# Kernel optimization log

Hardware: AMD Instinct MI355X
Metric: run time of the kernel (lower is better)

Reference implementation:

```python
import jax, jax.numpy as jnp
import numpy as np

N_USER = 100000
N_ITEM = 50000
N_NODES = N_USER + N_ITEM
LATDIM = 64
N_EDGES = 4800000
N_LAYERS = 3


def setup_inputs() -> dict:
    key = jax.random.key(0)
    k1, k2, k3, k4 = jax.random.split(key, 4)
    ini_embeds = jax.random.normal(k1, (N_NODES, LATDIM), dtype=jnp.float32)
    edge_src = jax.random.randint(k2, (N_EDGES,), 0, N_NODES, dtype=jnp.int32)
    edge_dst = jax.random.randint(k3, (N_EDGES,), 0, N_NODES, dtype=jnp.int32)
    edge_w = jax.random.uniform(k4, (N_EDGES,), dtype=jnp.float32)
    return {
        "ini_embeds": ini_embeds,
        "edge_src": edge_src,
        "edge_dst": edge_dst,
        "edge_w": edge_w,
        "n_user": N_USER,
        "n_layers": N_LAYERS,
    }


def _spmm(edge_src, edge_dst, edge_w, x, n_nodes):
    # out[dst] += w * x[src]  == adj @ x for sparse adj in COO form
    msgs = x[edge_src] * edge_w[:, None]  # [E, D]
    return jax.ops.segment_sum(msgs, edge_dst, num_segments=n_nodes)


def reference(ini_embeds, edge_src, edge_dst, edge_w, n_user, n_layers):
    n_nodes = ini_embeds.shape[0]
    embeds = ini_embeds
    acc = ini_embeds  # running sum of all layer embeddings (LightGCN layer sum)
    for _ in range(n_layers):
        embeds = _spmm(edge_src, edge_dst, edge_w, embeds, n_nodes)
        acc = acc + embeds
    return acc[:n_user], acc[n_user:]
```

## Files before the change

kernel.cpp:

```cpp
#include <hip/hip_runtime.h>
#include <hip/hip_fp16.h>


#define D 64
#define BSH 9
#define BW 512
#define PTILE 16384

__global__ void lg_zero_int(int* __restrict__ p, int n) {
    int i = blockIdx.x * blockDim.x + threadIdx.x;
    int st = gridDim.x * blockDim.x;
    for (; i < n; i += st) p[i] = 0;
}

__global__ void lg_f2h(const float* __restrict__ in, __half* __restrict__ out, int n4) {
    int i = blockIdx.x * blockDim.x + threadIdx.x;
    int st = gridDim.x * blockDim.x;
    const float4* src = (const float4*)in;
    uint2* dst = (uint2*)out;
    for (; i < n4; i += st) {
        float4 v = src[i];
        __half2 a = __floats2half2_rn(v.x, v.y);
        __half2 b = __floats2half2_rn(v.z, v.w);
        uint2 u;
        u.x = *reinterpret_cast<unsigned int*>(&a);
        u.y = *reinterpret_cast<unsigned int*>(&b);
        dst[i] = u;
    }
}

__global__ void lg_bhist(const int* __restrict__ edst, int* __restrict__ bcount,
                         int E, int NB) {
    extern __shared__ int lcnt[];
    for (int i = threadIdx.x; i < NB; i += blockDim.x) lcnt[i] = 0;
    __syncthreads();
    int i = blockIdx.x * blockDim.x + threadIdx.x;
    int st = gridDim.x * blockDim.x;
    for (; i < E; i += st) atomicAdd(&lcnt[edst[i] >> BSH], 1);
    __syncthreads();
    for (int j = threadIdx.x; j < NB; j += blockDim.x) {
        int v = lcnt[j];
        if (v) atomicAdd(&bcount[j], v);
    }
}

__global__ __launch_bounds__(1024) void lg_bscan(const int* counts, int* bptr, int* bcur,
                                                 int NB, int E, int* rowptr, int n_nodes) {
    __shared__ int lds[1024];
    int tid = threadIdx.x;
    int per = (NB + 1023) >> 10;
    int lo = tid * per; if (lo > NB) lo = NB;
    int hi = lo + per;  if (hi > NB) hi = NB;
    int sum = 0;
    for (int i = lo; i < hi; ++i) sum += counts[i];
    lds[tid] = sum;
    __syncthreads();
    for (int off = 1; off < 1024; off <<= 1) {
        int v = (tid >= off) ? lds[tid - off] : 0;
        __syncthreads();
        lds[tid] += v;
        __syncthreads();
    }
    int run = lds[tid] - sum;
    for (int i = lo; i < hi; ++i) {
        int c = counts[i];
        bptr[i] = run;
        bcur[i] = run;
        run += c;
    }
    if (tid == 0) { bptr[NB] = E; rowptr[n_nodes] = E; }
}

__global__ __launch_bounds__(256) void lg_part(const int* __restrict__ esrc,
                                               const int* __restrict__ edst,
                                               const float* __restrict__ ew,
                                               int* __restrict__ bcur,
                                               int2* __restrict__ bbuf,
                                               int E, int NB) {
    extern __shared__ int sm[];
    int* cnt = sm;
    int* base = sm + NB;
    int lo = blockIdx.x * PTILE;
    int hi = lo + PTILE; if (hi > E) hi = E;
    for (int i = threadIdx.x; i < NB; i += 256) cnt[i] = 0;
    __syncthreads();
    for (int i = lo + threadIdx.x; i < hi; i += 256)
        atomicAdd(&cnt[edst[i] >> BSH], 1);
    __syncthreads();
    for (int i = threadIdx.x; i < NB; i += 256) {
        int c = cnt[i];
        base[i] = c ? atomicAdd(&bcur[i], c) : 0;
        cnt[i] = 0;
    }
    __syncthreads();
    for (int i = lo + threadIdx.x; i < hi; i += 256) {
        int d = edst[i];
        int b = d >> BSH;
        int p = base[b] + atomicAdd(&cnt[b], 1);
        bbuf[p] = make_int2(esrc[i] | ((d & (BW - 1)) << 18), __float_as_int(ew[i]));
    }
}

__global__ __launch_bounds__(256) void lg_bfinal(const int2* __restrict__ bbuf,
                                                 const int* __restrict__ bptr,
                                                 int2* __restrict__ edata,
                                                 int* __restrict__ rowptr, int n_nodes) {
    __shared__ int cnt[BW];
    __shared__ int cur[BW];
    __shared__ int psum[256];
    int b = blockIdx.x;
    int s = bptr[b], e = bptr[b + 1];
    int tid = threadIdx.x;
    for (int i = tid; i < BW; i += 256) cnt[i] = 0;
    __syncthreads();
    for (int i = s + tid; i < e; i += 256)
        atomicAdd(&cnt[((unsigned)bbuf[i].x >> 18) & (BW - 1)], 1);
    __syncthreads();
    int c0 = cnt[2 * tid], c1 = cnt[2 * tid + 1];
    int mysum = c0 + c1;
    psum[tid] = mysum;
    __syncthreads();
    for (int off = 1; off < 256; off <<= 1) {
        int v = (tid >= off) ? psum[tid - off] : 0;
        __syncthreads();
        psum[tid] += v;
        __syncthreads();
    }
    int excl = psum[tid] - mysum;
    cur[2 * tid] = excl;
    cur[2 * tid + 1] = excl + c0;
    int node0 = b * BW + 2 * tid;
    if (node0 < n_nodes)     rowptr[node0]     = s + excl;
    if (node0 + 1 < n_nodes) rowptr[node0 + 1] = s + excl + c0;
    __syncthreads();
    for (int i = s + tid; i < e; i += 256) {
        int2 ed = bbuf[i];
        int loc = ((unsigned)ed.x >> 18) & (BW - 1);
        int p = s + atomicAdd(&cur[loc], 1);
        edata[p] = make_int2(ed.x & 0x3FFFF, ed.y);
    }
}

template <bool FIRST, bool LAST>
__global__ __launch_bounds__(256) void lg_gather(const int2* __restrict__ edata,
                                                 const int* __restrict__ rowptr,
                                                 const __half* __restrict__ x,
                                                 __half* __restrict__ y,
                                                 float* __restrict__ acc,
                                                 const float* __restrict__ ini,
                                                 int n_nodes) {
    int wid = (blockIdx.x * blockDim.x + threadIdx.x) >> 6;
    int lane = threadIdx.x & 63;
    if (wid >= n_nodes) return;
    int q = lane >> 4, c = lane & 15;
    int start = rowptr[wid], end = rowptr[wid + 1];
    float ax = 0.f, ay = 0.f, az = 0.f, aw = 0.f;
    int base = start;
    for (; base + 16 <= end; base += 16) {
        int2 e0 = edata[base + q];
        int2 e1 = edata[base + 4 + q];
        int2 e2 = edata[base + 8 + q];
        int2 e3 = edata[base + 12 + q];
        uint2 u0 = *((const uint2*)(x + (size_t)e0.x * D) + c);
        uint2 u1 = *((const uint2*)(x + (size_t)e1.x * D) + c);
        uint2 u2 = *((const uint2*)(x + (size_t)e2.x * D) + c);
        uint2 u3 = *((const uint2*)(x + (size_t)e3.x * D) + c);
        float w0 = __int_as_float(e0.y), w1 = __int_as_float(e1.y);
        float w2 = __int_as_float(e2.y), w3 = __int_as_float(e3.y);
        {
            float2 f0 = __half22float2(*reinterpret_cast<__half2*>(&u0.x));
            float2 f1 = __half22float2(*reinterpret_cast<__half2*>(&u0.y));
            ax += w0 * f0.x; ay += w0 * f0.y; az += w0 * f1.x; aw += w0 * f1.y;
        }
        {
            float2 f0 = __half22float2(*reinterpret_cast<__half2*>(&u1.x));
            float2 f1 = __half22float2(*reinterpret_cast<__half2*>(&u1.y));
            ax += w1 * f0.x; ay += w1 * f0.y; az += w1 * f1.x; aw += w1 * f1.y;
        }
        {
            float2 f0 = __half22float2(*reinterpret_cast<__half2*>(&u2.x));
            float2 f1 = __half22float2(*reinterpret_cast<__half2*>(&u2.y));
            ax += w2 * f0.x; ay += w2 * f0.y; az += w2 * f1.x; aw += w2 * f1.y;
        }
        {
            float2 f0 = __half22float2(*reinterpret_cast<__half2*>(&u3.x));
            float2 f1 = __half22float2(*reinterpret_cast<__half2*>(&u3.y));
            ax += w3 * f0.x; ay += w3 * f0.y; az += w3 * f1.x; aw += w3 * f1.y;
        }
    }
    for (; base < end; base += 4) {
        int idx = base + q;
        if (idx < end) {
            int2 e0 = edata[idx];
            float w0 = __int_as_float(e0.y);
            uint2 u0 = *((const uint2*)(x + (size_t)e0.x * D) + c);
            float2 f0 = __half22float2(*reinterpret_cast<__half2*>(&u0.x));
            float2 f1 = __half22float2(*reinterpret_cast<__half2*>(&u0.y));
            ax += w0 * f0.x; ay += w0 * f0.y; az += w0 * f1.x; aw += w0 * f1.y;
        }
    }
    ax += __shfl_xor(ax, 16); ax += __shfl_xor(ax, 32);
    ay += __shfl_xor(ay, 16); ay += __shfl_xor(ay, 32);
    az += __shfl_xor(az, 16); az += __shfl_xor(az, 32);
    aw += __shfl_xor(aw, 16); aw += __shfl_xor(aw, 32);
    if (lane < 16) {
        size_t o = (size_t)wid * D + (size_t)c * 4;
        if (!LAST) {
            __half2 h0 = __floats2half2_rn(ax, ay);
            __half2 h1 = __floats2half2_rn(az, aw);
            uint2 u;
            u.x = *reinterpret_cast<unsigned int*>(&h0);
            u.y = *reinterpret_cast<unsigned int*>(&h1);
            *(uint2*)(y + o) = u;
        }
        if (FIRST) {
            float4 iv = *(const float4*)(ini + o);
            *(float4*)(acc + o) = make_float4(iv.x + ax, iv.y + ay, iv.z + az, iv.w + aw);
        } else {
            float4 av = *(float4*)(acc + o);
            *(float4*)(acc + o) = make_float4(av.x + ax, av.y + ay, av.z + az, av.w + aw);
        }
    }
}

__global__ void lg_init_kernel(const float* __restrict__ ini, float* __restrict__ cur,
                               float* __restrict__ acc, float* __restrict__ nxt, int n4) {
    int i = blockIdx.x * blockDim.x + threadIdx.x;
    int stride = gridDim.x * blockDim.x;
    const float4* s = (const float4*)ini;
    float4* c = (float4*)cur; float4* a = (float4*)acc; float4* z = (float4*)nxt;
    float4 zero = make_float4(0.f, 0.f, 0.f, 0.f);
    for (; i < n4; i += stride) { float4 v = s[i]; c[i] = v; a[i] = v; z[i] = zero; }
}

__global__ void lg_spmm_kernel(const int* __restrict__ esrc, const int* __restrict__ edst,
                               const float* __restrict__ ew, const float* __restrict__ x,
                               float* __restrict__ y, int E) {
    int tid = blockIdx.x * blockDim.x + threadIdx.x;
    int e = tid >> 4;
    if (e >= E) return;
    int l = (tid & 15) << 2;
    int s = esrc[e]; int d = edst[e]; float w = ew[e];
    float4 v = *(const float4*)(x + s * D + l);
    float* yp = y + d * D + l;
    unsafeAtomicAdd(yp + 0, w * v.x);
    unsafeAtomicAdd(yp + 1, w * v.y);
    unsafeAtomicAdd(yp + 2, w * v.z);
    unsafeAtomicAdd(yp + 3, w * v.w);
}

__global__ void lg_addzero_kernel(float* __restrict__ acc, const float* __restrict__ nxt,
                                  float* __restrict__ zbuf, int n4) {
    int i = blockIdx.x * blockDim.x + threadIdx.x;
    int stride = gridDim.x * blockDim.x;
    float4* a = (float4*)acc; const float4* n = (const float4*)nxt; float4* z = (float4*)zbuf;
    float4 zero = make_float4(0.f, 0.f, 0.f, 0.f);
    for (; i < n4; i += stride) {
        float4 av = a[i]; float4 nv = n[i];
        av.x += nv.x; av.y += nv.y; av.z += nv.z; av.w += nv.w;
        a[i] = av; z[i] = zero;
    }
}

extern "C" void kernel_launch(void* const* d_in, const int* in_sizes, int n_in,
                              void* d_out, int out_size, void* d_ws, size_t ws_size,
                              hipStream_t stream) {
    const float* ini  = (const float*)d_in[0];
    const int*   esrc = (const int*)d_in[1];
    const int*   edst = (const int*)d_in[2];
    const float* ew   = (const float*)d_in[3];

    int n_nodes = in_sizes[0] / D;
    int E       = in_sizes[1];
    int NB      = (n_nodes + BW - 1) >> BSH;

    size_t hBytes     = ((size_t)n_nodes * D * sizeof(__half) + 255) & ~(size_t)255;
    size_t edataBytes = (size_t)E * sizeof(int2);
    size_t ptrBytes   = (((size_t)n_nodes + 1) * 4 + 15) & ~(size_t)15;
    size_t bptrBytes  = (((size_t)NB + 1) * 4 + 15) & ~(size_t)15;
    size_t need = 2 * hBytes + 2 * edataBytes + ptrBytes + bptrBytes + (size_t)NB * 4 + 64;

    float* acc = (float*)d_out;

    if (ws_size >= need) {
        char* p = (char*)d_ws;
        __half* h0    = (__half*)p; p += hBytes;
        __half* h1    = (__half*)p; p += hBytes;
        int2*  edata  = (int2*)p;   p += edataBytes;
        int2*  bbuf   = (int2*)p;   p += edataBytes;
        int*   rowptr = (int*)p;    p += ptrBytes;
        int*   bptr   = (int*)p;    p += bptrBytes;
        int*   bcur   = (int*)p;

        int ntiles = (E + PTILE - 1) / PTILE;
        int n4 = n_nodes * D / 4;

        lg_zero_int<<<(NB + 255) / 256, 256, 0, stream>>>(bcur, NB);
        lg_bhist<<<256, 256, (size_t)NB * 4, stream>>>(edst, bcur, E, NB);
        lg_bscan<<<1, 1024, 0, stream>>>(bcur, bptr, bcur, NB, E, rowptr, n_nodes);
        lg_part<<<ntiles, 256, (size_t)NB * 8, stream>>>(esrc, edst, ew, bcur, bbuf, E, NB);
        lg_f2h<<<2048, 256, 0, stream>>>(ini, h0, n4);
        lg_bfinal<<<NB, 256, 0, stream>>>(bbuf, bptr, edata, rowptr, n_nodes);

        int gblocks = (int)(((size_t)n_nodes * 64 + 255) / 256);
        lg_gather<true,  false><<<gblocks, 256, 0, stream>>>(edata, rowptr, h0, h1, acc, ini, n_nodes);
        lg_gather<false, false><<<gblocks, 256, 0, stream>>>(edata, rowptr, h1, h0, acc, ini, n_nodes);
        lg_gather<false, true ><<<gblocks, 256, 0, stream>>>(edata, rowptr, h0, h1, acc, ini, n_nodes);
    } else {
        int n4 = (n_nodes * D) / 4;
        float* cur = (float*)d_ws;
        float* nxt = cur + (size_t)n_nodes * D;
        lg_init_kernel<<<2048, 256, 0, stream>>>(ini, cur, acc, nxt, n4);
        int spmm_blocks = (E * 16 + 255) / 256;
        for (int layer = 0; layer < 3; ++layer) {
            lg_spmm_kernel<<<spmm_blocks, 256, 0, stream>>>(esrc, edst, ew, cur, nxt, E);
            lg_addzero_kernel<<<2048, 256, 0, stream>>>(acc, nxt, cur, n4);
            float* t = cur; cur = nxt; nxt = t;
        }
    }
}
```

Before: 487.7 us.

## Replace global-atomic bucket partition with per-tile histogram and flat scan

Rebuilds the CSR construction as a deterministic per-tile-per-bucket histogram, followed by one flat exclusive scan over an NB×ntiles table and a scatter that takes its offsets straight from that table. This removes the zeroing kernel, the global bucket-count atomics, and the per-tile global atomicAdd on bucket cursors. Block sizes go up to 1024 threads, and the final sort-within-bucket uses 512 scan lanes. In exchange, a single block must scan about 294×293 ≈ 86K entries, and the histogram table takes extra global memory traffic.

```diff
diff --git a/kernel.cpp b/kernel.cpp
--- a/kernel.cpp
+++ b/kernel.cpp
@@ -6,12 +6,6 @@
 #define BSH 9
 #define BW 512
 #define PTILE 16384
-
-__global__ void lg_zero_int(int* __restrict__ p, int n) {
-    int i = blockIdx.x * blockDim.x + threadIdx.x;
-    int st = gridDim.x * blockDim.x;
-    for (; i < n; i += st) p[i] = 0;
-}
 
 __global__ void lg_f2h(const float* __restrict__ in, __half* __restrict__ out, int n4) {
     int i = blockIdx.x * blockDim.x + threadIdx.x;
@@ -29,30 +23,33 @@
     }
 }
 
-__global__ void lg_bhist(const int* __restrict__ edst, int* __restrict__ bcount,
-                         int E, int NB) {
-    extern __shared__ int lcnt[];
-    for (int i = threadIdx.x; i < NB; i += blockDim.x) lcnt[i] = 0;
-    __syncthreads();
-    int i = blockIdx.x * blockDim.x + threadIdx.x;
-    int st = gridDim.x * blockDim.x;
-    for (; i < E; i += st) atomicAdd(&lcnt[edst[i] >> BSH], 1);
-    __syncthreads();
-    for (int j = threadIdx.x; j < NB; j += blockDim.x) {
-        int v = lcnt[j];
-        if (v) atomicAdd(&bcount[j], v);
-    }
-}
-
-__global__ __launch_bounds__(1024) void lg_bscan(const int* counts, int* bptr, int* bcur,
-                                                 int NB, int E, int* rowptr, int n_nodes) {
+__global__ __launch_bounds__(1024) void lg_tilehist(const int* __restrict__ edst,
+                                                    int* __restrict__ tcnt,
+                                                    int E, int NB, int ntiles) {
+    extern __shared__ int cnt[];
+    int t = blockIdx.x;
+    int lo = t * PTILE;
+    int hi = lo + PTILE; if (hi > E) hi = E;
+    for (int i = threadIdx.x; i < NB; i += 1024) cnt[i] = 0;
+    __syncthreads();
+    for (int i = lo + threadIdx.x; i < hi; i += 1024)
+        atomicAdd(&cnt[edst[i] >> BSH], 1);
+    __syncthreads();
+    for (int b = threadIdx.x; b < NB; b += 1024)
+        tcnt[b * ntiles + t] = cnt[b];
+}
+
+__global__ __launch_bounds__(1024) void lg_flatscan(const int* __restrict__ tcnt,
+                                                    int* __restrict__ tbase,
+                                                    int NT, int E,
+                                                    int* __restrict__ rowptr, int n_nodes) {
     __shared__ int lds[1024];
     int tid = threadIdx.x;
-    int per = (NB + 1023) >> 10;
-    int lo = tid * per; if (lo > NB) lo = NB;
-    int hi = lo + per;  if (hi > NB) hi = NB;
+    int per = (NT + 1023) >> 10;
+    int lo = tid * per; if (lo > NT) lo = NT;
+    int hi = lo + per;  if (hi > NT) hi = NT;
     int sum = 0;
-    for (int i = lo; i < hi; ++i) sum += counts[i];
+    for (int i = lo; i < hi; ++i) sum += tcnt[i];
     lds[tid] = sum;
     __syncthreads();
     for (int off = 1; off < 1024; off <<= 1) {
@@ -63,77 +60,66 @@
     }
     int run = lds[tid] - sum;
     for (int i = lo; i < hi; ++i) {
-        int c = counts[i];
-        bptr[i] = run;
-        bcur[i] = run;
-        run += c;
-    }
-    if (tid == 0) { bptr[NB] = E; rowptr[n_nodes] = E; }
-}
-
-__global__ __launch_bounds__(256) void lg_part(const int* __restrict__ esrc,
-                                               const int* __restrict__ edst,
-                                               const float* __restrict__ ew,
-                                               int* __restrict__ bcur,
-                                               int2* __restrict__ bbuf,
-                                               int E, int NB) {
-    extern __shared__ int sm[];
-    int* cnt = sm;
-    int* base = sm + NB;
-    int lo = blockIdx.x * PTILE;
+        tbase[i] = run;
+        run += tcnt[i];
+    }
+    if (tid == 0) rowptr[n_nodes] = E;
+}
+
+__global__ __launch_bounds__(1024) void lg_scatter2(const int* __restrict__ esrc,
+                                                    const int* __restrict__ edst,
+                                                    const float* __restrict__ ew,
+                                                    const int* __restrict__ tbase,
+                                                    int2* __restrict__ bbuf,
+                                                    int E, int NB, int ntiles) {
+    extern __shared__ int cur[];
+    int t = blockIdx.x;
+    int lo = t * PTILE;
     int hi = lo + PTILE; if (hi > E) hi = E;
-    for (int i = threadIdx.x; i < NB; i += 256) cnt[i] = 0;
-    __syncthreads();
-    for (int i = lo + threadIdx.x; i < hi; i += 256)
-        atomicAdd(&cnt[edst[i] >> BSH], 1);
-    __syncthreads();
-    for (int i = threadIdx.x; i < NB; i += 256) {
-        int c = cnt[i];
-        base[i] = c ? atomicAdd(&bcur[i], c) : 0;
-        cnt[i] = 0;
-    }
-    __syncthreads();
-    for (int i = lo + threadIdx.x; i < hi; i += 256) {
+    for (int b = threadIdx.x; b < NB; b += 1024) cur[b] = tbase[b * ntiles + t];
+    __syncthreads();
+    for (int i = lo + threadIdx.x; i < hi; i += 1024) {
         int d = edst[i];
         int b = d >> BSH;
-        int p = base[b] + atomicAdd(&cnt[b], 1);
+        int p = atomicAdd(&cur[b], 1);
         bbuf[p] = make_int2(esrc[i] | ((d & (BW - 1)) << 18), __float_as_int(ew[i]));
     }
 }
 
-__global__ __launch_bounds__(256) void lg_bfinal(const int2* __restrict__ bbuf,
-                                                 const int* __restrict__ bptr,
-                                                 int2* __restrict__ edata,
-                                                 int* __restrict__ rowptr, int n_nodes) {
+__global__ __launch_bounds__(1024) void lg_bfinal(const int2* __restrict__ bbuf,
+                                                  const int* __restrict__ tbase,
+                                                  int2* __restrict__ edata,
+                                                  int* __restrict__ rowptr,
+                                                  int n_nodes, int NB, int ntiles, int E) {
     __shared__ int cnt[BW];
     __shared__ int cur[BW];
-    __shared__ int psum[256];
+    __shared__ int psum[BW];
     int b = blockIdx.x;
-    int s = bptr[b], e = bptr[b + 1];
+    int s = tbase[b * ntiles];
+    int e = (b == NB - 1) ? E : tbase[(b + 1) * ntiles];
     int tid = threadIdx.x;
-    for (int i = tid; i < BW; i += 256) cnt[i] = 0;
-    __syncthreads();
-    for (int i = s + tid; i < e; i += 256)
+    if (tid < BW) cnt[tid] = 0;
+    __syncthreads();
+    for (int i = s + tid; i < e; i += 1024)
         atomicAdd(&cnt[((unsigned)bbuf[i].x >> 18) & (BW - 1)], 1);
     __syncthreads();
-    int c0 = cnt[2 * tid], c1 = cnt[2 * tid + 1];
-    int mysum = c0 + c1;
-    psum[tid] = mysum;
-    __syncthreads();
-    for (int off = 1; off < 256; off <<= 1) {
-        int v = (tid >= off) ? psum[tid - off] : 0;
+    if (tid < BW) psum[tid] = cnt[tid];
+    __syncthreads();
+    for (int off = 1; off < BW; off <<= 1) {
+        int v = 0;
+        if (tid < BW && tid >= off) v = psum[tid - off];
         __syncthreads();
-        psum[tid] += v;
+        if (tid < BW) psum[tid] += v;
         __syncthreads();
     }
-    int excl = psum[tid] - mysum;
-    cur[2 * tid] = excl;
-    cur[2 * tid + 1] = excl + c0;
-    int node0 = b * BW + 2 * tid;
-    if (node0 < n_nodes)     rowptr[node0]     = s + excl;
-    if (node0 + 1 < n_nodes) rowptr[node0 + 1] = s + excl + c0;
-    __syncthreads();
-    for (int i = s + tid; i < e; i += 256) {
+    if (tid < BW) {
+        int excl = psum[tid] - cnt[tid];
+        cur[tid] = excl;
+        int node = b * BW + tid;
+        if (node < n_nodes) rowptr[node] = s + excl;
+    }
+    __syncthreads();
+    for (int i = s + tid; i < e; i += 1024) {
         int2 ed = bbuf[i];
         int loc = ((unsigned)ed.x >> 18) & (BW - 1);
         int p = s + atomicAdd(&cur[loc], 1);
@@ -273,12 +259,14 @@
     int n_nodes = in_sizes[0] / D;
     int E       = in_sizes[1];
     int NB      = (n_nodes + BW - 1) >> BSH;
+    int ntiles  = (E + PTILE - 1) / PTILE;
+    int NT      = NB * ntiles;
 
     size_t hBytes     = ((size_t)n_nodes * D * sizeof(__half) + 255) & ~(size_t)255;
     size_t edataBytes = (size_t)E * sizeof(int2);
     size_t ptrBytes   = (((size_t)n_nodes + 1) * 4 + 15) & ~(size_t)15;
-    size_t bptrBytes  = (((size_t)NB + 1) * 4 + 15) & ~(size_t)15;
-    size_t need = 2 * hBytes + 2 * edataBytes + ptrBytes + bptrBytes + (size_t)NB * 4 + 64;
+    size_t tcntBytes  = (((size_t)NT * 4) + 15) & ~(size_t)15;
+    size_t need = 2 * hBytes + 2 * edataBytes + ptrBytes + 2 * tcntBytes + 64;
 
     float* acc = (float*)d_out;
 
@@ -289,18 +277,16 @@
         int2*  edata  = (int2*)p;   p += edataBytes;
         int2*  bbuf   = (int2*)p;   p += edataBytes;
         int*   rowptr = (int*)p;    p += ptrBytes;
-        int*   bptr   = (int*)p;    p += bptrBytes;
-        int*   bcur   = (int*)p;
-
-        int ntiles = (E + PTILE - 1) / PTILE;
+        int*   tcnt   = (int*)p;    p += tcntBytes;
+        int*   tbase  = (int*)p;
+
         int n4 = n_nodes * D / 4;
 
-        lg_zero_int<<<(NB + 255) / 256, 256, 0, stream>>>(bcur, NB);
-        lg_bhist<<<256, 256, (size_t)NB * 4, stream>>>(edst, bcur, E, NB);
-        lg_bscan<<<1, 1024, 0, stream>>>(bcur, bptr, bcur, NB, E, rowptr, n_nodes);
-        lg_part<<<ntiles, 256, (size_t)NB * 8, stream>>>(esrc, edst, ew, bcur, bbuf, E, NB);
         lg_f2h<<<2048, 256, 0, stream>>>(ini, h0, n4);
-        lg_bfinal<<<NB, 256, 0, stream>>>(bbuf, bptr, edata, rowptr, n_nodes);
+        lg_tilehist<<<ntiles, 1024, (size_t)NB * 4, stream>>>(edst, tcnt, E, NB, ntiles);
+        lg_flatscan<<<1, 1024, 0, stream>>>(tcnt, tbase, NT, E, rowptr, n_nodes);
+        lg_scatter2<<<ntiles, 1024, (size_t)NB * 4, stream>>>(esrc, edst, ew, tbase, bbuf, E, NB, ntiles);
+        lg_bfinal<<<NB, 1024, 0, stream>>>(bbuf, tbase, edata, rowptr, n_nodes, NB, ntiles, E);
 
         int gblocks = (int)(((size_t)n_nodes * 64 + 255) / 256);
         lg_gather<true,  false><<<gblocks, 256, 0, stream>>>(edata, rowptr, h0, h1, acc, ini, n_nodes);
```

Result: slower. 552.8 us (+13.4%).
